# Kernel optimization log

Measured on AMD Instinct MI355X. Metric: run time of the kernel, lower is better.

The kernel has to match this reference:

```python
import jax, jax.numpy as jnp
import numpy as np

B, S, D_IN, D_OUT = 4096, 200, 256, 128
NORM_FACT = 1.0 / np.sqrt(D_OUT).astype(np.float32)


def setup_inputs() -> dict:
    key = jax.random.key(0)
    k1, k2, k3, k4, k5, k6 = jax.random.split(key, 6)
    s = 1.0 / np.sqrt(D_IN).astype(np.float32)
    return {
        "x": jax.random.normal(k1, (B, S, D_IN), dtype=jnp.float32),
        "Q": jax.random.normal(k2, (B, 1, D_OUT), dtype=jnp.float32),
        "Wk": jax.random.normal(k3, (D_IN, D_OUT), dtype=jnp.float32) * s,
        "bk": jax.random.normal(k4, (D_OUT,), dtype=jnp.float32) * s,
        "Wv": jax.random.normal(k5, (D_IN, D_OUT), dtype=jnp.float32) * s,
        "bv": jax.random.normal(k6, (D_OUT,), dtype=jnp.float32) * s,
    }


def reference(x, Q, Wk, bk, Wv, bv):
    # x: [B,S,D_in], Q: [B,1,D_out]
    K = jnp.einsum("bsi,io->bso", x, Wk) + bk          # [B,S,d]
    V = jnp.einsum("bsi,io->bso", x, Wv) + bv          # [B,S,d]
    scores = jnp.einsum("btd,bsd->bts", Q, K)          # [B,1,S]
    # NOTE: scale applied AFTER softmax, faithful to the source module.
    atten = jax.nn.softmax(scores, axis=-1) * NORM_FACT  # [B,1,S]
    # V * atten.permute(0,2,1) -> [B,S,d] * [B,S,1], then sum over S
    output = jnp.sum(V * jnp.swapaxes(atten, 1, 2), axis=1)  # [B,d]
    return (output, atten)
```

## Files before the change

### kernel.cpp

```cpp
#include <hip/hip_runtime.h>
#include <math.h>

#define BB   4096
#define SS   200
#define DIN  256
#define DOUT 128

static constexpr float NORM_FACT = 0.08838834764831845f;

__global__ void wk_transpose_kernel(const float* __restrict__ Wk,
                                    float* __restrict__ WkT) {
    int idx = blockIdx.x * blockDim.x + threadIdx.x;
    if (idx < DIN * DOUT) {
        int i = idx & (DIN - 1);
        int o = idx >> 8;
        WkT[o * DIN + i] = Wk[i * DOUT + o];
    }
}

__global__ __launch_bounds__(256, 4)
void precompute_kernel(const float* __restrict__ Q,
                       const float* __restrict__ WkT,
                       const float* __restrict__ bk,
                       float* __restrict__ qkAll,
                       float2* __restrict__ params) {
    __shared__ float Qs[16][DOUT];
    __shared__ float bkS[DOUT];
    __shared__ float qkS[16][257];

    const int tid = threadIdx.x;
    const int bs  = blockIdx.x * 16;

    for (int i = tid; i < 16 * DOUT; i += 256)
        Qs[i >> 7][i & (DOUT - 1)] = Q[(size_t)bs * DOUT + i];
    if (tid < DOUT) bkS[tid] = bk[tid];
    __syncthreads();

    float acc[16];
    #pragma unroll
    for (int bb = 0; bb < 16; ++bb) acc[bb] = 0.0f;

    #pragma unroll 4
    for (int o = 0; o < DOUT; ++o) {
        const float wv = WkT[o * DIN + tid];
        #pragma unroll
        for (int bb = 0; bb < 16; ++bb) acc[bb] += wv * Qs[bb][o];
    }

    #pragma unroll
    for (int bb = 0; bb < 16; ++bb) {
        qkAll[(size_t)(bs + bb) * DIN + tid] = acc[bb];
        qkS[bb][tid] = acc[bb];
    }
    __syncthreads();

    const int b2 = tid >> 4, j = tid & 15;
    float sq = 0.0f;
    #pragma unroll
    for (int c = 0; c < 16; ++c) { const float v = qkS[b2][j * 16 + c]; sq += v * v; }
    float qb = 0.0f;
    #pragma unroll
    for (int c = 0; c < 8; ++c) qb += Qs[b2][j * 8 + c] * bkS[j * 8 + c];
    #pragma unroll
    for (int off = 1; off < 16; off <<= 1) {
        sq += __shfl_xor(sq, off, 64);
        qb += __shfl_xor(qb, off, 64);
    }
    if (j == 0) params[bs + b2] = make_float2(qb, qb + 5.0f * sqrtf(sq));
}

template<int NB>
__device__ __forceinline__ void process_batch(const float* __restrict__ row0,
                                              const float4 qv, const float qbm0,
                                              float& l, float4& acc,
                                              float* __restrict__ ew,
                                              const int lane) {
    float4 v[NB];
    #pragma unroll
    for (int j = 0; j < NB; ++j)
        v[j] = *reinterpret_cast<const float4*>(row0 + j * DIN);

    float e[NB];
    #pragma unroll
    for (int j = 0; j < NB; ++j) {
        float p = v[j].x * qv.x + v[j].y * qv.y + v[j].z * qv.z + v[j].w * qv.w;
        p += __shfl_xor(p, 1,  64);
        p += __shfl_xor(p, 2,  64);
        p += __shfl_xor(p, 4,  64);
        p += __shfl_xor(p, 8,  64);
        p += __shfl_xor(p, 16, 64);
        p += __shfl_xor(p, 32, 64);
        e[j] = __expf(p + qbm0);
    }

    #pragma unroll
    for (int j = 0; j < NB; ++j) {
        l += e[j];
        acc.x += e[j] * v[j].x; acc.y += e[j] * v[j].y;
        acc.z += e[j] * v[j].z; acc.w += e[j] * v[j].w;
    }
    if (lane == 0) {
        #pragma unroll
        for (int j = 0; j < NB; ++j) ew[j] = e[j];
    }
}

__global__ __launch_bounds__(256, 4)
void attn_stream_kernel(const float* __restrict__ x,
                        const float* __restrict__ qkAll,
                        const float2* __restrict__ params,
                        float* __restrict__ accAll,
                        float* __restrict__ out_a) {
    __shared__ float eS[SS];
    __shared__ float accW[4][DIN];
    __shared__ float lW[4];

    const int b    = blockIdx.x;
    const int tid  = threadIdx.x;
    const int w    = tid >> 6;
    const int lane = tid & 63;

    const float2 pb = params[b];
    const float qbm0 = pb.x - pb.y;

    const float4 qv = *reinterpret_cast<const float4*>(
        qkAll + (size_t)b * DIN + lane * 4);

    const int sBeg = w * 50;
    const float* rbase = x + (size_t)b * SS * DIN + (size_t)sBeg * DIN + lane * 4;

    float  l = 0.0f;
    float4 acc = make_float4(0.0f, 0.0f, 0.0f, 0.0f);

    #pragma unroll 1
    for (int t = 0; t < 48; t += 8)
        process_batch<8>(rbase + t * DIN, qv, qbm0, l, acc, &eS[sBeg + t], lane);
    process_batch<2>(rbase + 48 * DIN, qv, qbm0, l, acc, &eS[sBeg + 48], lane);

    accW[w][lane * 4 + 0] = acc.x;
    accW[w][lane * 4 + 1] = acc.y;
    accW[w][lane * 4 + 2] = acc.z;
    accW[w][lane * 4 + 3] = acc.w;
    if (lane == 0) lW[w] = l;
    __syncthreads();

    const float lf  = lW[0] + lW[1] + lW[2] + lW[3];
    const float inv = NORM_FACT / lf;

    if (tid < SS)
        out_a[(size_t)b * SS + tid] = eS[tid] * inv;

    accAll[(size_t)b * DIN + tid] =
        (accW[0][tid] + accW[1][tid] + accW[2][tid] + accW[3][tid]) * inv;
}

__global__ __launch_bounds__(256, 4)
void proj_kernel(const float* __restrict__ accAll,
                 const float* __restrict__ Wv,
                 const float* __restrict__ bv,
                 float* __restrict__ out_o) {
    __shared__ float accS[2][DIN];
    const int tid = threadIdx.x;
    const int bb  = tid >> 7;
    const int o   = tid & (DOUT - 1);
    const int b0  = blockIdx.x * 2;

    #pragma unroll
    for (int i = tid; i < 2 * DIN; i += 256)
        accS[i >> 8][i & (DIN - 1)] = accAll[(size_t)b0 * DIN + i];
    __syncthreads();

    float pacc = 0.0f;
    #pragma unroll 8
    for (int r = 0; r < DIN; ++r)
        pacc += accS[bb][r] * Wv[r * DOUT + o];

    out_o[(size_t)(b0 + bb) * DOUT + o] = pacc + NORM_FACT * bv[o];
}

extern "C" void kernel_launch(void* const* d_in, const int* in_sizes, int n_in,
                              void* d_out, int out_size, void* d_ws, size_t ws_size,
                              hipStream_t stream) {
    const float* x  = (const float*)d_in[0];
    const float* Q  = (const float*)d_in[1];
    const float* Wk = (const float*)d_in[2];
    const float* bk = (const float*)d_in[3];
    const float* Wv = (const float*)d_in[4];
    const float* bv = (const float*)d_in[5];

    float* out   = (float*)d_out;
    float* out_o = out;
    float* out_a = out + (size_t)BB * DOUT;

    float*  WkT    = (float*)d_ws;
    float*  qkAll  = WkT + DIN * DOUT;
    float2* params = (float2*)(qkAll + (size_t)BB * DIN);
    float*  accAll = (float*)(params + BB);

    wk_transpose_kernel<<<(DIN * DOUT + 255) / 256, 256, 0, stream>>>(Wk, WkT);
    precompute_kernel<<<BB / 16, 256, 0, stream>>>(Q, WkT, bk, qkAll, params);
    attn_stream_kernel<<<BB, 256, 0, stream>>>(x, qkAll, params, accAll, out_a);
    proj_kernel<<<BB / 2, 256, 0, stream>>>(accAll, Wv, bv, out_o);
}
```

Baseline: 199.1 us.

## Fuse value projection into attention streaming kernel and raise occupancy

```diff
diff --git a/kernel.cpp b/kernel.cpp
--- a/kernel.cpp
+++ b/kernel.cpp
@@ -105,15 +105,19 @@
     }
 }
 
-__global__ __launch_bounds__(256, 4)
-void attn_stream_kernel(const float* __restrict__ x,
-                        const float* __restrict__ qkAll,
-                        const float2* __restrict__ params,
-                        float* __restrict__ accAll,
-                        float* __restrict__ out_a) {
+__global__ __launch_bounds__(256, 8)
+void attn_fused_kernel(const float* __restrict__ x,
+                       const float* __restrict__ qkAll,
+                       const float2* __restrict__ params,
+                       const float* __restrict__ Wv,
+                       const float* __restrict__ bv,
+                       float* __restrict__ out_o,
+                       float* __restrict__ out_a) {
     __shared__ float eS[SS];
     __shared__ float accW[4][DIN];
     __shared__ float lW[4];
+    __shared__ float accF[DIN];
+    __shared__ float part[2][DOUT];
 
     const int b    = blockIdx.x;
     const int tid  = threadIdx.x;
@@ -133,8 +137,8 @@
     float4 acc = make_float4(0.0f, 0.0f, 0.0f, 0.0f);
 
     #pragma unroll 1
-    for (int t = 0; t < 48; t += 8)
-        process_batch<8>(rbase + t * DIN, qv, qbm0, l, acc, &eS[sBeg + t], lane);
+    for (int t = 0; t < 48; t += 4)
+        process_batch<4>(rbase + t * DIN, qv, qbm0, l, acc, &eS[sBeg + t], lane);
     process_batch<2>(rbase + 48 * DIN, qv, qbm0, l, acc, &eS[sBeg + 48], lane);
 
     accW[w][lane * 4 + 0] = acc.x;
@@ -150,32 +154,25 @@
     if (tid < SS)
         out_a[(size_t)b * SS + tid] = eS[tid] * inv;
 
-    accAll[(size_t)b * DIN + tid] =
-        (accW[0][tid] + accW[1][tid] + accW[2][tid] + accW[3][tid]) * inv;
-}
-
-__global__ __launch_bounds__(256, 4)
-void proj_kernel(const float* __restrict__ accAll,
-                 const float* __restrict__ Wv,
-                 const float* __restrict__ bv,
-                 float* __restrict__ out_o) {
-    __shared__ float accS[2][DIN];
-    const int tid = threadIdx.x;
-    const int bb  = tid >> 7;
-    const int o   = tid & (DOUT - 1);
-    const int b0  = blockIdx.x * 2;
-
-    #pragma unroll
-    for (int i = tid; i < 2 * DIN; i += 256)
-        accS[i >> 8][i & (DIN - 1)] = accAll[(size_t)b0 * DIN + i];
-    __syncthreads();
-
-    float pacc = 0.0f;
-    #pragma unroll 8
-    for (int r = 0; r < DIN; ++r)
-        pacc += accS[bb][r] * Wv[r * DOUT + o];
-
-    out_o[(size_t)(b0 + bb) * DOUT + o] = pacc + NORM_FACT * bv[o];
+    accF[tid] = (accW[0][tid] + accW[1][tid] + accW[2][tid] + accW[3][tid]) * inv;
+    __syncthreads();
+
+    {
+        const int o = tid & (DOUT - 1);
+        const int h = tid >> 7;
+        float pacc = 0.0f;
+        #pragma unroll 8
+        for (int i = 0; i < DIN / 2; ++i) {
+            const int r = h * (DIN / 2) + i;
+            pacc += accF[r] * Wv[r * DOUT + o];
+        }
+        part[h][o] = pacc;
+    }
+    __syncthreads();
+
+    if (tid < DOUT)
+        out_o[(size_t)b * DOUT + tid] =
+            part[0][tid] + part[1][tid] + NORM_FACT * bv[tid];
 }
 
 extern "C" void kernel_launch(void* const* d_in, const int* in_sizes, int n_in,
@@ -195,10 +192,9 @@
     float*  WkT    = (float*)d_ws;
     float*  qkAll  = WkT + DIN * DOUT;
     float2* params = (float2*)(qkAll + (size_t)BB * DIN);
-    float*  accAll = (float*)(params + BB);
 
     wk_transpose_kernel<<<(DIN * DOUT + 255) / 256, 256, 0, stream>>>(Wk, WkT);
     precompute_kernel<<<BB / 16, 256, 0, stream>>>(Q, WkT, bk, qkAll, params);
-    attn_stream_kernel<<<BB, 256, 0, stream>>>(x, qkAll, params, accAll, out_a);
-    proj_kernel<<<BB / 2, 256, 0, stream>>>(accAll, Wv, bv, out_o);
-}
+    attn_fused_kernel<<<BB, 256, 0, stream>>>(x, qkAll, params, Wv, bv,
+                                              out_o, out_a);
+}
```

New measurement: 183.8 us. -7.6%, faster.
